# Optimization experiments

Measured on AMD Instinct MI355X. Metric: run time of the kernel, lower is better.

## Reference

```python
import jax, jax.numpy as jnp
import numpy as np

IN_DIM = 256
NUM_HEADS = 8
HEAD_DIM = IN_DIM // NUM_HEADS


def setup_inputs() -> dict:
    key = jax.random.key(0)
    k1, k2, k3, k4, k5, k6 = jax.random.split(key, 6)
    B, C, H, W = 2, IN_DIM, 64, 64
    scale = 1.0 / np.sqrt(IN_DIM)
    return {
        "tgt": jax.random.normal(k1, (B, C, H, W), dtype=jnp.float32),
        "src": jax.random.normal(k2, (B, C, H, W), dtype=jnp.float32),
        # nn.Linear weights stored as [out, in] (torch convention); y = x @ W.T
        "Wq": jax.random.normal(k3, (IN_DIM, IN_DIM), dtype=jnp.float32) * scale,
        "Wk": jax.random.normal(k4, (IN_DIM, IN_DIM), dtype=jnp.float32) * scale,
        "Wv": jax.random.normal(k5, (IN_DIM, IN_DIM), dtype=jnp.float32) * scale,
        "Wo": jax.random.normal(k6, (IN_DIM, IN_DIM), dtype=jnp.float32) * scale,
    }


def reference(tgt, src, Wq, Wk, Wv, Wo):
    B, C, H, W = src.shape
    N = H * W
    # b c h w -> b (h w) c
    src_t = src.reshape(B, C, N).transpose(0, 2, 1)
    tgt_t = tgt.reshape(B, C, N).transpose(0, 2, 1)
    # project and split heads: [B, N, C] -> [B, heads, N, head_dim]
    def heads(x, Wt):
        y = jnp.einsum('bnc,dc->bnd', x, Wt)
        return y.reshape(B, N, NUM_HEADS, HEAD_DIM).transpose(0, 2, 1, 3)
    q = heads(tgt_t, Wq)
    k = heads(src_t, Wk)
    v = heads(src_t, Wv)
    scores = jnp.einsum('bhqd,bhkd->bhqk', q, k) / jnp.sqrt(jnp.float32(HEAD_DIM))
    attn = jax.nn.softmax(scores, axis=-1)
    weighted = jnp.einsum('bhqk,bhkd->bhqd', attn, v)  # [B, heads, N, head_dim]
    weighted = weighted.transpose(0, 2, 1, 3).reshape(B, N, C)
    out = jnp.einsum('bnc,dc->bnd', weighted + tgt_t, Wo)
    return out
```

## Files before the change

kernel.cpp:

```cpp
#include <hip/hip_runtime.h>
#include <hip/hip_bf16.h>

#define IN_DIM 256
#define NHEADS 8
#define HDIM 32
#define BATCH 2
#define NTOK 4096
#define QSCALE (0.17677669529663687f * 1.4426950408889634f)

typedef __hip_bfloat16 bf16;
typedef __attribute__((ext_vector_type(8))) short bf16x8;
typedef __attribute__((ext_vector_type(4))) short bf16x4;
typedef __attribute__((ext_vector_type(4))) float f32x4;

union bfrag { bf16x8 v; bf16x4 h[2]; };

__device__ __forceinline__ float b2f(bf16 x) { return __bfloat162float(x); }

#if __has_builtin(__builtin_amdgcn_exp2f)
__device__ __forceinline__ float fast_exp2(float x) { return __builtin_amdgcn_exp2f(x); }
#else
__device__ __forceinline__ float fast_exp2(float x) { return exp2f(x); }
#endif

__device__ __forceinline__ unsigned packbf2(float a, float b) {
    union { __hip_bfloat162 h; unsigned u; } c;
    c.h = __float22bfloat162_rn(float2{a, b});
    return c.u;
}

__device__ __forceinline__ void pack16(float4 a, float4 b, float4 c, float4 d,
                                       bf16* dst) {
    uint2 w0 = {packbf2(a.x, a.y), packbf2(a.z, a.w)};
    uint2 w1 = {packbf2(b.x, b.y), packbf2(b.z, b.w)};
    uint2 w2 = {packbf2(c.x, c.y), packbf2(c.z, c.w)};
    uint2 w3 = {packbf2(d.x, d.y), packbf2(d.z, d.w)};
    *(uint2*)(dst + 0)  = w0;
    *(uint2*)(dst + 4)  = w1;
    *(uint2*)(dst + 8)  = w2;
    *(uint2*)(dst + 12) = w3;
}

__global__ __launch_bounds__(256) void proj_mfma(
    const float* __restrict__ tgt, const float* __restrict__ src,
    const float* __restrict__ Wq, const float* __restrict__ Wk,
    const float* __restrict__ Wv,
    bf16* __restrict__ Qo, bf16* __restrict__ Ko, bf16* __restrict__ Vo)
{
    const int which = blockIdx.y;
    const int dh = blockIdx.z;
    const int b  = blockIdx.x >> 7;
    const int n0 = (blockIdx.x & 127) * 32;
    const float* X = (which == 0) ? tgt : src;
    const float* W = (which == 0) ? Wq : (which == 1 ? Wk : Wv);

    const int tid = threadIdx.x;
    const int wave = tid >> 6, lane = tid & 63;
    const int lg = lane >> 4, lc = lane & 15;
    const int wn = wave & 1, wdq = wave >> 1;

    __shared__ bf16 As[32 * 260];
    __shared__ bf16 Ws[2][128 * 36];

    {
        const float* Xb = X + (size_t)b * IN_DIM * NTOK + n0;
        for (int it = 0; it < 8; ++it) {
            int idx = it * 256 + tid;
            int c = idx >> 3, j4 = idx & 7;
            float4 x = *(const float4*)(Xb + (size_t)c * NTOK + j4 * 4);
            As[(j4 * 4 + 0) * 260 + c] = __float2bfloat16(x.x);
            As[(j4 * 4 + 1) * 260 + c] = __float2bfloat16(x.y);
            As[(j4 * 4 + 2) * 260 + c] = __float2bfloat16(x.z);
            As[(j4 * 4 + 3) * 260 + c] = __float2bfloat16(x.w);
        }
    }
    const int wd = tid >> 1, wc = (tid & 1) * 16;
    const float* Wbase = W + (size_t)(dh * 128 + wd) * IN_DIM + wc;
    {
        float4 a = *(const float4*)(Wbase + 0);
        float4 bb = *(const float4*)(Wbase + 4);
        float4 cc = *(const float4*)(Wbase + 8);
        float4 dd = *(const float4*)(Wbase + 12);
        pack16(a, bb, cc, dd, &Ws[0][wd * 36 + wc]);
    }
    __syncthreads();

    f32x4 acc[4];
    #pragma unroll
    for (int t = 0; t < 4; ++t) acc[t] = f32x4{0.f, 0.f, 0.f, 0.f};

    for (int s = 0; s < 8; ++s) {
        const int c0 = s * 32;
        float4 pa, pb, pc, pd;
        if (s < 7) {
            const float* wn_ = Wbase + (s + 1) * 32;
            pa = *(const float4*)(wn_ + 0);
            pb = *(const float4*)(wn_ + 4);
            pc = *(const float4*)(wn_ + 8);
            pd = *(const float4*)(wn_ + 12);
        }
        bfrag af;
        const bf16* ap = &As[(wn * 16 + lc) * 260 + c0 + lg * 8];
        af.h[0] = *(const bf16x4*)ap;
        af.h[1] = *(const bf16x4*)(ap + 4);
        #pragma unroll
        for (int t = 0; t < 4; ++t) {
            bfrag wf;
            const bf16* wp = &Ws[s & 1][(wdq * 64 + t * 16 + lc) * 36 + lg * 8];
            wf.h[0] = *(const bf16x4*)wp;
            wf.h[1] = *(const bf16x4*)(wp + 4);
            acc[t] = __builtin_amdgcn_mfma_f32_16x16x32_bf16(af.v, wf.v, acc[t], 0, 0, 0);
        }
        if (s < 7) {
            __syncthreads();
            pack16(pa, pb, pc, pd, &Ws[(s + 1) & 1][wd * 36 + wc]);
            __syncthreads();
        }
    }

    const int nb = n0 + wn * 16 + lg * 4;
    if (which == 2) {
        #pragma unroll
        for (int t = 0; t < 4; ++t) {
            int d = dh * 128 + wdq * 64 + t * 16 + lc;
            uint2 pk;
            pk.x = packbf2(acc[t][0], acc[t][1]);
            pk.y = packbf2(acc[t][2], acc[t][3]);
            *(uint2*)(Vo + ((size_t)b * IN_DIM + d) * NTOK + nb) = pk;
        }
    } else {
        const float sc = (which == 0) ? QSCALE : 1.0f;
        bf16* O = (which == 0) ? Qo : Ko;
        #pragma unroll
        for (int t = 0; t < 4; ++t)
            #pragma unroll
            for (int r = 0; r < 4; ++r)
                O[((size_t)b * NTOK + nb + r) * IN_DIM + dh * 128 + wdq * 64 + t * 16 + lc]
                    = __float2bfloat16(acc[t][r] * sc);
    }
}

#define KLSZ (64 * 40)
#define VLSZ (32 * 72)
__global__ __launch_bounds__(512) void attn_mfma_kernel(
    const bf16* __restrict__ Q, const bf16* __restrict__ K,
    const bf16* __restrict__ Vt, const float* __restrict__ tgt,
    bf16* __restrict__ Wt)
{
    const int blk = blockIdx.x;
    const int bh  = 2 * (blk & 7) + ((blk >> 3) & 1);
    const int qb  = blk >> 4;
    const int b = bh >> 3, h = bh & 7;
    const int tid  = threadIdx.x;
    const int wave = tid >> 6;
    const int grp  = wave >> 2;
    const int wl   = wave & 3;
    const int lane = tid & 63;
    const int lg = lane >> 4, lc = lane & 15;
    const int qw = qb * 128 + wl * 32;

    __shared__ __align__(16) char pool[4 * KLSZ * 2 + 4 * VLSZ * 2];
    bf16* KLb = (bf16*)pool;
    bf16* VLb = (bf16*)(pool + 4 * KLSZ * 2);
    float* redC = (float*)pool;

    const bf16x8 qfa = *(const bf16x8*)(Q + ((size_t)b * NTOK + qw + lc) * IN_DIM
                                          + h * HDIM + lg * 8);
    const bf16x8 qfb = *(const bf16x8*)(Q + ((size_t)b * NTOK + qw + 16 + lc) * IN_DIM
                                          + h * HDIM + lg * 8);

    bf16x8 ones8;
    #pragma unroll
    for (int i = 0; i < 8; ++i) ((short*)&ones8)[i] = (short)0x3F80;
    const f32x4 z = {0.f, 0.f, 0.f, 0.f};

    const int tg   = tid & 255;
    const int srow = tg >> 2, sd = (tg & 3) * 8;
    const int vrow = tg >> 3, vch = tg & 7;
    const int kwoff = grp * 2 * KLSZ + srow * 40 + sd;
    const int vwoff = grp * 2 * VLSZ + vrow * 72 + vch * 8;
    const int kroff = grp * 2 * KLSZ + lc * 40 + lg * 8;
    const int vroff0 = grp * 2 * VLSZ + lc * 72 + lg * 4;
    const int vroff1 = grp * 2 * VLSZ + (16 + lc) * 72 + lg * 4;

    const bf16* Kp = K  + ((size_t)b * NTOK + grp * 2048 + srow) * IN_DIM + h * HDIM + sd;
    const bf16* Vp = Vt + ((size_t)b * IN_DIM + h * HDIM + vrow) * NTOK + grp * 2048 + vch * 8;

    f32x4 o0a = {0.f,0.f,0.f,0.f}, o1a = {0.f,0.f,0.f,0.f}, ola = {0.f,0.f,0.f,0.f};
    f32x4 o0b = {0.f,0.f,0.f,0.f}, o1b = {0.f,0.f,0.f,0.f}, olb = {0.f,0.f,0.f,0.f};

    bf16x8 kreg = *(const bf16x8*)Kp;
    bf16x8 vreg = *(const bf16x8*)Vp;
    Kp += (size_t)64 * IN_DIM;
    Vp += 64;

#define HALF(CUR)                                                              \
    {                                                                          \
        *(bf16x8*)&KLb[kwoff + (CUR) * KLSZ] = kreg;                           \
        *(bf16x8*)&VLb[vwoff + (CUR) * VLSZ] = vreg;                           \
        kreg = *(const bf16x8*)Kp;                                             \
        vreg = *(const bf16x8*)Vp;                                             \
        Kp += (size_t)64 * IN_DIM;                                             \
        Vp += 64;                                                              \
        __syncthreads();                                                       \
        bf16x8 kf[4];                                                          \
        _Pragma("unroll")                                                      \
        for (int t = 0; t < 4; ++t)                                            \
            kf[t] = *(const bf16x8*)&KLb[kroff + (CUR) * KLSZ + t * 640];      \
        bf16x4 v0[4], v1[4];                                                   \
        _Pragma("unroll")                                                      \
        for (int t = 0; t < 4; ++t) {                                          \
            v0[t] = *(const bf16x4*)&VLb[vroff0 + (CUR) * VLSZ + t * 16];      \
            v1[t] = *(const bf16x4*)&VLb[vroff1 + (CUR) * VLSZ + t * 16];      \
        }                                                                      \
        f32x4 sa[4], sb[4];                                                    \
        __builtin_amdgcn_s_setprio(1);                                         \
        _Pragma("unroll")                                                      \
        for (int t = 0; t < 4; ++t) {                                          \
            sa[t] = __builtin_amdgcn_mfma_f32_16x16x32_bf16(kf[t], qfa, z, 0,0,0); \
            sb[t] = __builtin_amdgcn_mfma_f32_16x16x32_bf16(kf[t], qfb, z, 0,0,0); \
        }                                                                      \
        __builtin_amdgcn_s_setprio(0);                                         \
        _Pragma("unroll")                                                      \
        for (int tcp = 0; tcp < 2; ++tcp) {                                    \
            union { bf16x8 v; uint4 u; } pa, pb;                               \
            pa.u.x = packbf2(fast_exp2(sa[2*tcp][0]),   fast_exp2(sa[2*tcp][1]));   \
            pa.u.y = packbf2(fast_exp2(sa[2*tcp][2]),   fast_exp2(sa[2*tcp][3]));   \
            pa.u.z = packbf2(fast_exp2(sa[2*tcp+1][0]), fast_exp2(sa[2*tcp+1][1])); \
            pa.u.w = packbf2(fast_exp2(sa[2*tcp+1][2]), fast_exp2(sa[2*tcp+1][3])); \
            pb.u.x = packbf2(fast_exp2(sb[2*tcp][0]),   fast_exp2(sb[2*tcp][1]));   \
            pb.u.y = packbf2(fast_exp2(sb[2*tcp][2]),   fast_exp2(sb[2*tcp][3]));   \
            pb.u.z = packbf2(fast_exp2(sb[2*tcp+1][0]), fast_exp2(sb[2*tcp+1][1])); \
            pb.u.w = packbf2(fast_exp2(sb[2*tcp+1][2]), fast_exp2(sb[2*tcp+1][3])); \
            bfrag B0, B1;                                                      \
            B0.h[0] = v0[2*tcp]; B0.h[1] = v0[2*tcp+1];                        \
            B1.h[0] = v1[2*tcp]; B1.h[1] = v1[2*tcp+1];                        \
            __builtin_amdgcn_s_setprio(1);                                     \
            o0a = __builtin_amdgcn_mfma_f32_16x16x32_bf16(pa.v, B0.v, o0a, 0,0,0); \
            o1a = __builtin_amdgcn_mfma_f32_16x16x32_bf16(pa.v, B1.v, o1a, 0,0,0); \
            ola = __builtin_amdgcn_mfma_f32_16x16x32_bf16(pa.v, ones8, ola, 0,0,0); \
            o0b = __builtin_amdgcn_mfma_f32_16x16x32_bf16(pb.v, B0.v, o0b, 0,0,0); \
            o1b = __builtin_amdgcn_mfma_f32_16x16x32_bf16(pb.v, B1.v, o1b, 0,0,0); \
            olb = __builtin_amdgcn_mfma_f32_16x16x32_bf16(pb.v, ones8, olb, 0,0,0); \
            __builtin_amdgcn_s_setprio(0);                                     \
        }                                                                      \
    }

    for (int it = 0; it < NTOK / 256; ++it) {
        HALF(0)
        HALF(1)
    }
#undef HALF

    __syncthreads();
    if (grp) {
        float* d = &redC[(wl * 64 + lane) * 24];
        *(f32x4*)(d + 0)  = o0a;  *(f32x4*)(d + 4)  = o1a;  *(f32x4*)(d + 8)  = ola;
        *(f32x4*)(d + 12) = o0b;  *(f32x4*)(d + 16) = o1b;  *(f32x4*)(d + 20) = olb;
    }
    __syncthreads();
    if (!grp) {
        const float* s = &redC[(wl * 64 + lane) * 24];
        o0a += *(const f32x4*)(s + 0);
        o1a += *(const f32x4*)(s + 4);
        ola += *(const f32x4*)(s + 8);
        o0b += *(const f32x4*)(s + 12);
        o1b += *(const f32x4*)(s + 16);
        olb += *(const f32x4*)(s + 20);

        const float* tga = tgt + ((size_t)b * IN_DIM + h * HDIM + lc) * NTOK + qw + lg * 4;
        float4 r0a = *(const float4*)tga;
        float4 r1a = *(const float4*)(tga + (size_t)16 * NTOK);
        float4 r0b = *(const float4*)(tga + 16);
        float4 r1b = *(const float4*)(tga + (size_t)16 * NTOK + 16);

        bf16* opa = Wt + ((size_t)b * NTOK + qw + lg * 4) * IN_DIM + h * HDIM + lc;
        bf16* opb = opa + (size_t)16 * IN_DIM;
        #pragma unroll
        for (int r = 0; r < 4; ++r) {
            float inva = 1.f / ola[r];
            float invb = 1.f / olb[r];
            opa[(size_t)r * IN_DIM]      = __float2bfloat16(o0a[r] * inva + (&r0a.x)[r]);
            opa[(size_t)r * IN_DIM + 16] = __float2bfloat16(o1a[r] * inva + (&r1a.x)[r]);
            opb[(size_t)r * IN_DIM]      = __float2bfloat16(o0b[r] * invb + (&r0b.x)[r]);
            opb[(size_t)r * IN_DIM + 16] = __float2bfloat16(o1b[r] * invb + (&r1b.x)[r]);
        }
    }
}
#undef KLSZ
#undef VLSZ

__global__ __launch_bounds__(256) void out_mfma(
    const bf16* __restrict__ A, const float* __restrict__ Wo,
    float* __restrict__ out)
{
    const int dh = blockIdx.y;
    const int b  = blockIdx.x >> 7;
    const int n0 = (blockIdx.x & 127) * 32;

    const int tid = threadIdx.x;
    const int wave = tid >> 6, lane = tid & 63;
    const int lg = lane >> 4, lc = lane & 15;
    const int wn = wave & 1, wdq = wave >> 1;

    __shared__ bf16 As[32 * 260];
    __shared__ bf16 Ws[2][128 * 36];

    {
        const bf16* Ab = A + ((size_t)b * NTOK + n0) * IN_DIM;
        for (int it = 0; it < 4; ++it) {
            int idx = it * 256 + tid;
            int r = idx >> 5, ch = idx & 31;
            bfrag v;
            v.v = *(const bf16x8*)(Ab + (size_t)r * IN_DIM + ch * 8);
            *(bf16x4*)&As[r * 260 + ch * 8]     = v.h[0];
            *(bf16x4*)&As[r * 260 + ch * 8 + 4] = v.h[1];
        }
    }
    const int wd = tid >> 1, wc = (tid & 1) * 16;
    const float* Wbase = Wo + (size_t)(dh * 128 + wd) * IN_DIM + wc;
    {
        float4 a = *(const float4*)(Wbase + 0);
        float4 bb = *(const float4*)(Wbase + 4);
        float4 cc = *(const float4*)(Wbase + 8);
        float4 dd = *(const float4*)(Wbase + 12);
        pack16(a, bb, cc, dd, &Ws[0][wd * 36 + wc]);
    }
    __syncthreads();

    f32x4 acc[4];
    #pragma unroll
    for (int t = 0; t < 4; ++t) acc[t] = f32x4{0.f, 0.f, 0.f, 0.f};

    for (int s = 0; s < 8; ++s) {
        const int c0 = s * 32;
        float4 pa, pb, pc, pd;
        if (s < 7) {
            const float* wn_ = Wbase + (s + 1) * 32;
            pa = *(const float4*)(wn_ + 0);
            pb = *(const float4*)(wn_ + 4);
            pc = *(const float4*)(wn_ + 8);
            pd = *(const float4*)(wn_ + 12);
        }
        bfrag af;
        const bf16* ap = &As[(wn * 16 + lc) * 260 + c0 + lg * 8];
        af.h[0] = *(const bf16x4*)ap;
        af.h[1] = *(const bf16x4*)(ap + 4);
        #pragma unroll
        for (int t = 0; t < 4; ++t) {
            bfrag wf;
            const bf16* wp = &Ws[s & 1][(wdq * 64 + t * 16 + lc) * 36 + lg * 8];
            wf.h[0] = *(const bf16x4*)wp;
            wf.h[1] = *(const bf16x4*)(wp + 4);
            acc[t] = __builtin_amdgcn_mfma_f32_16x16x32_bf16(af.v, wf.v, acc[t], 0, 0, 0);
        }
        if (s < 7) {
            __syncthreads();
            pack16(pa, pb, pc, pd, &Ws[(s + 1) & 1][wd * 36 + wc]);
            __syncthreads();
        }
    }

    const int nb = n0 + wn * 16 + lg * 4;
    #pragma unroll
    for (int t = 0; t < 4; ++t)
        #pragma unroll
        for (int r = 0; r < 4; ++r)
            out[((size_t)b * NTOK + nb + r) * IN_DIM + dh * 128 + wdq * 64 + t * 16 + lc]
                = acc[t][r];
}

extern "C" void kernel_launch(void* const* d_in, const int* in_sizes, int n_in,
                              void* d_out, int out_size, void* d_ws, size_t ws_size,
                              hipStream_t stream) {
    const float* tgt = (const float*)d_in[0];
    const float* src = (const float*)d_in[1];
    const float* Wq  = (const float*)d_in[2];
    const float* Wk  = (const float*)d_in[3];
    const float* Wv  = (const float*)d_in[4];
    const float* Wo  = (const float*)d_in[5];
    float* out = (float*)d_out;

    const size_t SZ = (size_t)BATCH * NTOK * IN_DIM * sizeof(bf16);
    char* w = (char*)d_ws;
    bf16* Qb  = (bf16*)(w);
    bf16* Kb  = (bf16*)(w + SZ);
    bf16* Vtb = (bf16*)(w + 2 * SZ);
    bf16* Wt  = (bf16*)(w + 3 * SZ);

    proj_mfma<<<dim3(256, 3, 2), 256, 0, stream>>>(tgt, src, Wq, Wk, Wv, Qb, Kb, Vtb);

    attn_mfma_kernel<<<512, 512, 0, stream>>>(Qb, Kb, Vtb, tgt, Wt);

    out_mfma<<<dim3(256, 2), 256, 0, stream>>>(Wt, Wo, out);
}
```

Baseline: 83.55 us.

## Widen projection GEMM tiles to all 256 output columns per block

The Q/K/V projection and output projection kernels each now compute all 256 output features per block instead of splitting them across two blocks. The input token tile is therefore loaded and converted once rather than twice. Each wave keeps eight accumulator tiles and each thread streams a full 32-wide slice of one weight row into a doubled LDS buffer. The first barrier in the double-buffered loop is also removed. The grid is halved, which lowers parallelism and raises register and LDS use per block, and the barrier removal needs the buffer alternation to be race-free.

```diff
diff --git a/kernel.cpp b/kernel.cpp
--- a/kernel.cpp
+++ b/kernel.cpp
@@ -48,7 +48,6 @@
     bf16* __restrict__ Qo, bf16* __restrict__ Ko, bf16* __restrict__ Vo)
 {
     const int which = blockIdx.y;
-    const int dh = blockIdx.z;
     const int b  = blockIdx.x >> 7;
     const int n0 = (blockIdx.x & 127) * 32;
     const float* X = (which == 0) ? tgt : src;
@@ -60,7 +59,7 @@
     const int wn = wave & 1, wdq = wave >> 1;
 
     __shared__ bf16 As[32 * 260];
-    __shared__ bf16 Ws[2][128 * 36];
+    __shared__ bf16 Ws[2][256 * 36];
 
     {
         const float* Xb = X + (size_t)b * IN_DIM * NTOK + n0;
@@ -74,46 +73,47 @@
             As[(j4 * 4 + 3) * 260 + c] = __float2bfloat16(x.w);
         }
     }
-    const int wd = tid >> 1, wc = (tid & 1) * 16;
-    const float* Wbase = W + (size_t)(dh * 128 + wd) * IN_DIM + wc;
+    const float* Wrow = W + (size_t)tid * IN_DIM;
     {
-        float4 a = *(const float4*)(Wbase + 0);
-        float4 bb = *(const float4*)(Wbase + 4);
-        float4 cc = *(const float4*)(Wbase + 8);
-        float4 dd = *(const float4*)(Wbase + 12);
-        pack16(a, bb, cc, dd, &Ws[0][wd * 36 + wc]);
+        float4 q0 = *(const float4*)(Wrow + 0);
+        float4 q1 = *(const float4*)(Wrow + 4);
+        float4 q2 = *(const float4*)(Wrow + 8);
+        float4 q3 = *(const float4*)(Wrow + 12);
+        float4 q4 = *(const float4*)(Wrow + 16);
+        float4 q5 = *(const float4*)(Wrow + 20);
+        float4 q6 = *(const float4*)(Wrow + 24);
+        float4 q7 = *(const float4*)(Wrow + 28);
+        pack16(q0, q1, q2, q3, &Ws[0][tid * 36]);
+        pack16(q4, q5, q6, q7, &Ws[0][tid * 36 + 16]);
     }
     __syncthreads();
 
-    f32x4 acc[4];
+    f32x4 acc[8];
     #pragma unroll
-    for (int t = 0; t < 4; ++t) acc[t] = f32x4{0.f, 0.f, 0.f, 0.f};
+    for (int t = 0; t < 8; ++t) acc[t] = f32x4{0.f, 0.f, 0.f, 0.f};
 
     for (int s = 0; s < 8; ++s) {
-        const int c0 = s * 32;
-        float4 pa, pb, pc, pd;
+        float4 p[8];
         if (s < 7) {
-            const float* wn_ = Wbase + (s + 1) * 32;
-            pa = *(const float4*)(wn_ + 0);
-            pb = *(const float4*)(wn_ + 4);
-            pc = *(const float4*)(wn_ + 8);
-            pd = *(const float4*)(wn_ + 12);
+            const float* wnx = Wrow + (s + 1) * 32;
+            #pragma unroll
+            for (int i = 0; i < 8; ++i) p[i] = *(const float4*)(wnx + i * 4);
         }
         bfrag af;
-        const bf16* ap = &As[(wn * 16 + lc) * 260 + c0 + lg * 8];
+        const bf16* ap = &As[(wn * 16 + lc) * 260 + s * 32 + lg * 8];
         af.h[0] = *(const bf16x4*)ap;
         af.h[1] = *(const bf16x4*)(ap + 4);
         #pragma unroll
-        for (int t = 0; t < 4; ++t) {
+        for (int t = 0; t < 8; ++t) {
             bfrag wf;
-            const bf16* wp = &Ws[s & 1][(wdq * 64 + t * 16 + lc) * 36 + lg * 8];
+            const bf16* wp = &Ws[s & 1][(wdq * 128 + t * 16 + lc) * 36 + lg * 8];
             wf.h[0] = *(const bf16x4*)wp;
             wf.h[1] = *(const bf16x4*)(wp + 4);
             acc[t] = __builtin_amdgcn_mfma_f32_16x16x32_bf16(af.v, wf.v, acc[t], 0, 0, 0);
         }
         if (s < 7) {
-            __syncthreads();
-            pack16(pa, pb, pc, pd, &Ws[(s + 1) & 1][wd * 36 + wc]);
+            pack16(p[0], p[1], p[2], p[3], &Ws[(s + 1) & 1][tid * 36]);
+            pack16(p[4], p[5], p[6], p[7], &Ws[(s + 1) & 1][tid * 36 + 16]);
             __syncthreads();
         }
     }
@@ -121,8 +121,8 @@
     const int nb = n0 + wn * 16 + lg * 4;
     if (which == 2) {
         #pragma unroll
-        for (int t = 0; t < 4; ++t) {
-            int d = dh * 128 + wdq * 64 + t * 16 + lc;
+        for (int t = 0; t < 8; ++t) {
+            int d = wdq * 128 + t * 16 + lc;
             uint2 pk;
             pk.x = packbf2(acc[t][0], acc[t][1]);
             pk.y = packbf2(acc[t][2], acc[t][3]);
@@ -132,10 +132,10 @@
         const float sc = (which == 0) ? QSCALE : 1.0f;
         bf16* O = (which == 0) ? Qo : Ko;
         #pragma unroll
-        for (int t = 0; t < 4; ++t)
+        for (int t = 0; t < 8; ++t)
             #pragma unroll
             for (int r = 0; r < 4; ++r)
-                O[((size_t)b * NTOK + nb + r) * IN_DIM + dh * 128 + wdq * 64 + t * 16 + lc]
+                O[((size_t)b * NTOK + nb + r) * IN_DIM + wdq * 128 + t * 16 + lc]
                     = __float2bfloat16(acc[t][r] * sc);
     }
 }
@@ -294,7 +294,6 @@
     const bf16* __restrict__ A, const float* __restrict__ Wo,
     float* __restrict__ out)
 {
-    const int dh = blockIdx.y;
     const int b  = blockIdx.x >> 7;
     const int n0 = (blockIdx.x & 127) * 32;
 
@@ -304,7 +303,7 @@
     const int wn = wave & 1, wdq = wave >> 1;
 
     __shared__ bf16 As[32 * 260];
-    __shared__ bf16 Ws[2][128 * 36];
+    __shared__ bf16 Ws[2][256 * 36];
 
     {
         const bf16* Ab = A + ((size_t)b * NTOK + n0) * IN_DIM;
@@ -317,56 +316,57 @@
             *(bf16x4*)&As[r * 260 + ch * 8 + 4] = v.h[1];
         }
     }
-    const int wd = tid >> 1, wc = (tid & 1) * 16;
-    const float* Wbase = Wo + (size_t)(dh * 128 + wd) * IN_DIM + wc;
+    const float* Wrow = Wo + (size_t)tid * IN_DIM;
     {
-        float4 a = *(const float4*)(Wbase + 0);
-        float4 bb = *(const float4*)(Wbase + 4);
-        float4 cc = *(const float4*)(Wbase + 8);
-        float4 dd = *(const float4*)(Wbase + 12);
-        pack16(a, bb, cc, dd, &Ws[0][wd * 36 + wc]);
+        float4 q0 = *(const float4*)(Wrow + 0);
+        float4 q1 = *(const float4*)(Wrow + 4);
+        float4 q2 = *(const float4*)(Wrow + 8);
+        float4 q3 = *(const float4*)(Wrow + 12);
+        float4 q4 = *(const float4*)(Wrow + 16);
+        float4 q5 = *(const float4*)(Wrow + 20);
+        float4 q6 = *(const float4*)(Wrow + 24);
+        float4 q7 = *(const float4*)(Wrow + 28);
+        pack16(q0, q1, q2, q3, &Ws[0][tid * 36]);
+        pack16(q4, q5, q6, q7, &Ws[0][tid * 36 + 16]);
     }
     __syncthreads();
 
-    f32x4 acc[4];
+    f32x4 acc[8];
     #pragma unroll
-    for (int t = 0; t < 4; ++t) acc[t] = f32x4{0.f, 0.f, 0.f, 0.f};
+    for (int t = 0; t < 8; ++t) acc[t] = f32x4{0.f, 0.f, 0.f, 0.f};
 
     for (int s = 0; s < 8; ++s) {
-        const int c0 = s * 32;
-        float4 pa, pb, pc, pd;
+        float4 p[8];
         if (s < 7) {
-            const float* wn_ = Wbase + (s + 1) * 32;
-            pa = *(const float4*)(wn_ + 0);
-            pb = *(const float4*)(wn_ + 4);
-            pc = *(const float4*)(wn_ + 8);
-            pd = *(const float4*)(wn_ + 12);
+            const float* wnx = Wrow + (s + 1) * 32;
+            #pragma unroll
+            for (int i = 0; i < 8; ++i) p[i] = *(const float4*)(wnx + i * 4);
         }
         bfrag af;
-        const bf16* ap = &As[(wn * 16 + lc) * 260 + c0 + lg * 8];
+        const bf16* ap = &As[(wn * 16 + lc) * 260 + s * 32 + lg * 8];
         af.h[0] = *(const bf16x4*)ap;
         af.h[1] = *(const bf16x4*)(ap + 4);
         #pragma unroll
-        for (int t = 0; t < 4; ++t) {
+        for (int t = 0; t < 8; ++t) {
             bfrag wf;
-            const bf16* wp = &Ws[s & 1][(wdq * 64 + t * 16 + lc) * 36 + lg * 8];
+            const bf16* wp = &Ws[s & 1][(wdq * 128 + t * 16 + lc) * 36 + lg * 8];
             wf.h[0] = *(const bf16x4*)wp;
             wf.h[1] = *(const bf16x4*)(wp + 4);
             acc[t] = __builtin_amdgcn_mfma_f32_16x16x32_bf16(af.v, wf.v, acc[t], 0, 0, 0);
         }
         if (s < 7) {
-            __syncthreads();
-            pack16(pa, pb, pc, pd, &Ws[(s + 1) & 1][wd * 36 + wc]);
+            pack16(p[0], p[1], p[2], p[3], &Ws[(s + 1) & 1][tid * 36]);
+            pack16(p[4], p[5], p[6], p[7], &Ws[(s + 1) & 1][tid * 36 + 16]);
             __syncthreads();
         }
     }
 
     const int nb = n0 + wn * 16 + lg * 4;
     #pragma unroll
-    for (int t = 0; t < 4; ++t)
+    for (int t = 0; t < 8; ++t)
         #pragma unroll
         for (int r = 0; r < 4; ++r)
-            out[((size_t)b * NTOK + nb + r) * IN_DIM + dh * 128 + wdq * 64 + t * 16 + lc]
+            out[((size_t)b * NTOK + nb + r) * IN_DIM + wdq * 128 + t * 16 + lc]
                 = acc[t][r];
 }
 
@@ -388,9 +388,9 @@
     bf16* Vtb = (bf16*)(w + 2 * SZ);
     bf16* Wt  = (bf16*)(w + 3 * SZ);
 
-    proj_mfma<<<dim3(256, 3, 2), 256, 0, stream>>>(tgt, src, Wq, Wk, Wv, Qb, Kb, Vtb);
+    proj_mfma<<<dim3(BATCH * 128, 3), 256, 0, stream>>>(tgt, src, Wq, Wk, Wv, Qb, Kb, Vtb);
 
     attn_mfma_kernel<<<512, 512, 0, stream>>>(Qb, Kb, Vtb, tgt, Wt);
 
-    out_mfma<<<dim3(256, 2), 256, 0, stream>>>(Wt, Wo, out);
-}
+    out_mfma<<<BATCH * 128, 256, 0, stream>>>(Wt, Wo, out);
+}
```

Result: slower. 98.68 us (+18.1%).
